# Optimization experiments

Measured on AMD Instinct MI355X. Metric: run time of the kernel, lower is better.

The kernel has to match this reference:

```python
import jax, jax.numpy as jnp
import numpy as np

EPS = 1e-12  # matches torch F.normalize default eps (clamp_min)
B, C, N = 32, 512, 4096
K_CLUSTERS, G_CLUSTERS = 64, 8
T_CLUSTERS = K_CLUSTERS + G_CLUSTERS  # 72
H_ATTN = T_CLUSTERS // 4  # 18


def _l2norm(v, axis):
    return v / jnp.maximum(jnp.linalg.norm(v, axis=axis, keepdims=True), EPS)


def setup_inputs() -> dict:
    key = jax.random.key(0)
    ks = jax.random.split(key, 6)
    x = jax.random.normal(ks[0], (B, C, N), dtype=jnp.float32)
    centroids = jax.random.normal(ks[1], (T_CLUSTERS, C), dtype=jnp.float32) * 0.01
    # 1x1 Conv2d(C -> T) == dense [T, C] weight + bias
    conv_w = jax.random.normal(ks[2], (T_CLUSTERS, C), dtype=jnp.float32) / np.sqrt(C).astype(np.float32)
    conv_b = jnp.zeros((T_CLUSTERS,), dtype=jnp.float32)
    ghost_weights = jnp.ones((G_CLUSTERS,), dtype=jnp.float32) * 0.1
    w1 = jax.random.normal(ks[3], (H_ATTN, T_CLUSTERS), dtype=jnp.float32) / np.sqrt(T_CLUSTERS).astype(np.float32)
    b1 = jnp.zeros((H_ATTN,), dtype=jnp.float32)
    w2 = jax.random.normal(ks[4], (T_CLUSTERS, H_ATTN), dtype=jnp.float32) / np.sqrt(H_ATTN).astype(np.float32)
    b2 = jnp.zeros((T_CLUSTERS,), dtype=jnp.float32)
    return {"x": x, "centroids": centroids, "conv_w": conv_w, "conv_b": conv_b,
            "ghost_weights": ghost_weights, "w1": w1, "b1": b1, "w2": w2, "b2": b2}


def reference(x, centroids, conv_w, conv_b, ghost_weights, w1, b1, w2, b2):
    # x: [B, C, N] -> L2 normalize over channel dim
    xn = _l2norm(x, axis=1)
    # 1x1 conv -> soft assignment logits [B, T, N], softmax over clusters
    logits = jnp.einsum('kc,bcn->bkn', conv_w, xn) + conv_b[None, :, None]
    assign = jax.nn.softmax(logits, axis=1)
    # residual aggregation, algebraically fused:
    # vlad[b,k,c] = sum_n a[b,k,n]*x[b,c,n] - centroid[k,c]*sum_n a[b,k,n]
    agg = jnp.einsum('bkn,bcn->bkc', assign, xn)
    mass = assign.sum(axis=-1)  # [B, T]
    vlad = agg - centroids[None, :, :] * mass[:, :, None]
    # ghost cluster down-weighting
    gw = jax.nn.softmax(ghost_weights)
    vlad = vlad.at[:, K_CLUSTERS:, :].multiply(gw[None, :, None])
    # attention over clusters: mean over C -> MLP -> softmax over clusters
    scores = vlad.mean(axis=-1)  # [B, T]
    h = jax.nn.relu(scores @ w1.T + b1)
    attn = jax.nn.softmax(h @ w2.T + b2, axis=1)
    vlad = vlad * attn[:, :, None]
    # intra-cluster L2 norm, drop ghosts, flatten, global L2 norm
    vlad = _l2norm(vlad, axis=2)
    vlad = vlad[:, :K_CLUSTERS, :].reshape(vlad.shape[0], -1)
    return _l2norm(vlad, axis=1)
```

## Files before the change

kernel.cpp:

```cpp
#include <hip/hip_runtime.h>
#include <hip/hip_bf16.h>

#define B_ 32
#define C_ 512
#define N_ 4096
#define T_ 72
#define K_ 64
#define KP 80
#define EPSF 1e-12f

typedef unsigned short u16;
typedef unsigned int u32;
typedef __attribute__((ext_vector_type(8))) short bf16x8;
typedef __attribute__((ext_vector_type(4))) float f32x4;

__device__ __forceinline__ u16 f2bf(float v) {
    __hip_bfloat16 h = __float2bfloat16(v);
    return *reinterpret_cast<u16*>(&h);
}

__global__ __launch_bounds__(256) void k_prep(
    const float* __restrict__ conv_w, const float* __restrict__ conv_b,
    u16* __restrict__ Wp, float* __restrict__ bp)
{
    const int idx = blockIdx.x * 256 + threadIdx.x;
    if (idx < KP * C_) {
        const int k = idx >> 9, c = idx & (C_ - 1);
        Wp[idx] = f2bf(k < T_ ? conv_w[k * C_ + c] : 0.f);
    } else if (idx < KP * C_ + KP) {
        const int j = idx - KP * C_;
        bp[j] = (j < T_) ? conv_b[j] : -1e30f;
    }
}

#define AN 64
#define ACH 256
__global__ __launch_bounds__(256) void k_assign(
    const float* __restrict__ x, const u16* __restrict__ Wp,
    const float* __restrict__ bp, u16* __restrict__ assignp,
    float* __restrict__ mass)
{
    __shared__ u16   xt[AN][264];
    __shared__ float red[AN][9];
    __shared__ float linv[AN];

    const int t  = threadIdx.x;
    const int b  = blockIdx.y;
    const int n0 = blockIdx.x * AN;

    const int np = t & 31;
    const int cg = t >> 5;
    const float* xb = x + (size_t)b * C_ * N_ + n0 + 2 * np;

    const int lane = t & 63, w = t >> 6;
    const int q = lane >> 4, nl = lane & 15;

    f32x4 acc[5];
    #pragma unroll
    for (int mt = 0; mt < 5; ++mt) acc[mt] = (f32x4)0.f;

    float ss0 = 0.f, ss1 = 0.f;

    #pragma unroll 1
    for (int half = 0; half < 2; ++half) {
        const int cbase = half * ACH;
        #pragma unroll 4
        for (int ci = 0; ci < 32; ++ci) {
            const int c = cg * 32 + ci;
            const float2 v = *(const float2*)(xb + (size_t)(cbase + c) * N_);
            ss0 = fmaf(v.x, v.x, ss0);
            ss1 = fmaf(v.y, v.y, ss1);
            xt[2 * np][c]     = f2bf(v.x);
            xt[2 * np + 1][c] = f2bf(v.y);
        }
        if (half == 1) {
            red[2 * np][cg]     = ss0;
            red[2 * np + 1][cg] = ss1;
        }
        __syncthreads();
        if (half == 1 && t < AN) {
            float s = 0.f;
            #pragma unroll
            for (int j = 0; j < 8; ++j) s += red[t][j];
            linv[t] = 1.0f / fmaxf(sqrtf(s), EPSF);
        }
        const u16* wrow = Wp + (size_t)nl * C_ + cbase + q * 8;
        #pragma unroll
        for (int ks = 0; ks < ACH / 32; ++ks) {
            const bf16x8 bf = *(const bf16x8*)(&xt[16 * w + nl][ks * 32 + q * 8]);
            #pragma unroll
            for (int mt = 0; mt < 5; ++mt) {
                const bf16x8 af = *(const bf16x8*)(wrow + (size_t)(mt * 16) * C_ + ks * 32);
                acc[mt] = __builtin_amdgcn_mfma_f32_16x16x32_bf16(af, bf, acc[mt], 0, 0, 0);
            }
        }
        __syncthreads();
    }

    const float invn  = linv[16 * w + nl];
    const int   nglob = n0 + 16 * w + nl;

    float lg[5][4];
    #pragma unroll
    for (int mt = 0; mt < 5; ++mt)
        #pragma unroll
        for (int r = 0; r < 4; ++r)
            lg[mt][r] = acc[mt][r] * invn + bp[mt * 16 + q * 4 + r];

    float mx = -1e30f;
    #pragma unroll
    for (int mt = 0; mt < 5; ++mt)
        #pragma unroll
        for (int r = 0; r < 4; ++r) mx = fmaxf(mx, lg[mt][r]);
    mx = fmaxf(mx, __shfl_xor(mx, 16, 64));
    mx = fmaxf(mx, __shfl_xor(mx, 32, 64));

    float s = 0.f;
    #pragma unroll
    for (int mt = 0; mt < 5; ++mt)
        #pragma unroll
        for (int r = 0; r < 4; ++r) {
            lg[mt][r] = __expf(lg[mt][r] - mx);
            s += lg[mt][r];
        }
    s += __shfl_xor(s, 16, 64);
    s += __shfl_xor(s, 32, 64);
    const float rs = 1.0f / s;

    #pragma unroll
    for (int mt = 0; mt < 4; ++mt)
        #pragma unroll
        for (int r = 0; r < 4; ++r) {
            const float a = lg[mt][r] * rs;
            float msum = a;
            msum += __shfl_xor(msum, 1, 64);
            msum += __shfl_xor(msum, 2, 64);
            msum += __shfl_xor(msum, 4, 64);
            msum += __shfl_xor(msum, 8, 64);
            const int k = mt * 16 + q * 4 + r;
            if (nl == 0) atomicAdd(&mass[b * K_ + k], msum);
            assignp[((size_t)b * K_ + k) * N_ + nglob] = f2bf(a * invn);
        }
}

#define GBK 64
#define NCH 4
__global__ __launch_bounds__(256) void k_agg(
    const float* __restrict__ x, const u16* __restrict__ assignp,
    float* __restrict__ out)
{
    __shared__ u16 At[K_][72];
    __shared__ u16 Bt[K_][72];

    const int t  = threadIdx.x;
    const int b  = blockIdx.z;
    const int nc0 = blockIdx.y * (N_ / NCH);
    const int c0  = blockIdx.x * 64;

    const int lane = t & 63, w = t >> 6;
    const int q = lane >> 4, nl = lane & 15;

    f32x4 acc[4];
    #pragma unroll
    for (int mt = 0; mt < 4; ++mt) acc[mt] = (f32x4)0.f;

    const u16*   ab = assignp + (size_t)b * K_ * N_;
    const float* xb = x + (size_t)b * C_ * N_;

    const int au = t & 7,  ar = t >> 3;
    const int bp2 = t & 31, bc = t >> 5;

    #pragma unroll 1
    for (int n0 = nc0; n0 < nc0 + N_ / NCH; n0 += GBK) {
        __syncthreads();
        #pragma unroll
        for (int p = 0; p < 2; ++p) {
            const int r = ar + 32 * p;
            *(uint4*)(&At[r][au * 8]) =
                *(const uint4*)(ab + (size_t)r * N_ + n0 + au * 8);
        }
        #pragma unroll
        for (int p = 0; p < 8; ++p) {
            const int c = bc + 8 * p;
            const float2 v = *(const float2*)(xb + (size_t)(c0 + c) * N_ + n0 + 2 * bp2);
            const u32 pk = (u32)f2bf(v.x) | ((u32)f2bf(v.y) << 16);
            *(u32*)(&Bt[c][2 * bp2]) = pk;
        }
        __syncthreads();
        #pragma unroll
        for (int kk = 0; kk < 2; ++kk) {
            const bf16x8 bf = *(const bf16x8*)(&Bt[16 * w + nl][kk * 32 + q * 8]);
            #pragma unroll
            for (int mt = 0; mt < 4; ++mt) {
                const bf16x8 af = *(const bf16x8*)(&At[mt * 16 + nl][kk * 32 + q * 8]);
                acc[mt] = __builtin_amdgcn_mfma_f32_16x16x32_bf16(af, bf, acc[mt], 0, 0, 0);
            }
        }
    }

    float* ob = out + (size_t)b * K_ * C_;
    const int c = c0 + 16 * w + nl;
    #pragma unroll
    for (int mt = 0; mt < 4; ++mt)
        #pragma unroll
        for (int r = 0; r < 4; ++r)
            atomicAdd(&ob[(size_t)(mt * 16 + q * 4 + r) * C_ + c], acc[mt][r]);
}

__device__ __forceinline__ float block_reduce_sum_256(float v) {
    #pragma unroll
    for (int o = 32; o > 0; o >>= 1) v += __shfl_down(v, o, 64);
    __shared__ float wsh[4];
    const int lane = threadIdx.x & 63, wid = threadIdx.x >> 6;
    if (lane == 0) wsh[wid] = v;
    __syncthreads();
    float r = 0.f;
    if (threadIdx.x == 0) r = wsh[0] + wsh[1] + wsh[2] + wsh[3];
    return r;
}

__global__ __launch_bounds__(256) void k_rnorm(
    const float* __restrict__ agg, const float* __restrict__ centroids,
    const float* __restrict__ mass, float* __restrict__ rnorm,
    float* __restrict__ gsum)
{
    const int k = blockIdx.x, b = blockIdx.y;
    const float mk = mass[b * K_ + k];
    const float* p  = agg + ((size_t)b * K_ + k) * C_;
    const float* cb = centroids + k * C_;
    float s = 0.f;
    #pragma unroll 2
    for (int i = threadIdx.x; i < C_; i += 256) {
        const float v = fmaf(-cb[i], mk, p[i]);
        s = fmaf(v, v, s);
    }
    const float ss = block_reduce_sum_256(s);
    if (threadIdx.x == 0) {
        const float rn = fmaxf(sqrtf(ss), EPSF);
        rnorm[b * K_ + k] = rn;
        atomicAdd(gsum + b, ss / (rn * rn));
    }
}

__global__ __launch_bounds__(256) void k_final(
    float* __restrict__ out, const float* __restrict__ centroids,
    const float* __restrict__ mass, const float* __restrict__ rnorm,
    const float* __restrict__ gsum)
{
    const size_t i4 = ((size_t)blockIdx.x * 256 + threadIdx.x) * 4;
    const int b = (int)(i4 >> 15);
    const int k = (int)((i4 >> 9) & 63);
    const int c = (int)(i4 & 511);
    const float gn = fmaxf(sqrtf(gsum[b]), EPSF);
    const float sc = 1.0f / (rnorm[b * K_ + k] * gn);
    const float mk = mass[b * K_ + k];
    float4 v  = *(const float4*)(out + i4);
    const float4 cv = *(const float4*)(centroids + k * C_ + c);
    v.x = fmaf(-cv.x, mk, v.x) * sc;
    v.y = fmaf(-cv.y, mk, v.y) * sc;
    v.z = fmaf(-cv.z, mk, v.z) * sc;
    v.w = fmaf(-cv.w, mk, v.w) * sc;
    *(float4*)(out + i4) = v;
}

extern "C" void kernel_launch(void* const* d_in, const int* in_sizes, int n_in,
                              void* d_out, int out_size, void* d_ws, size_t ws_size,
                              hipStream_t stream) {
    const float* x         = (const float*)d_in[0];
    const float* centroids = (const float*)d_in[1];
    const float* conv_w    = (const float*)d_in[2];
    const float* conv_b    = (const float*)d_in[3];

    float* out = (float*)d_out;
    char*  ws  = (char*)d_ws;

    u16*   assignp = (u16*)ws;
    u16*   Wp      = (u16*)(ws + 16777216);
    float* bpad    = (float*)(ws + 16777216 + 81920);
    float* mass    = (float*)(ws + 16777216 + 81920 + 320);
    float* rnorm   = mass + B_ * K_;
    float* gsum    = rnorm + B_ * K_;

    hipMemsetAsync(mass, 0, B_ * K_ * sizeof(float), stream);
    hipMemsetAsync(gsum, 0, B_ * sizeof(float), stream);
    hipMemsetAsync(out, 0, (size_t)out_size * sizeof(float), stream);

    k_prep<<<dim3((KP * C_ + KP + 255) / 256), 256, 0, stream>>>(conv_w, conv_b, Wp, bpad);
    k_assign<<<dim3(N_ / AN, B_), 256, 0, stream>>>(x, Wp, bpad, assignp, mass);
    k_agg<<<dim3(C_ / 64, NCH, B_), 256, 0, stream>>>(x, assignp, out);
    k_rnorm<<<dim3(K_, B_), 256, 0, stream>>>(out, centroids, mass, rnorm, gsum);
    k_final<<<(out_size / 4 + 255) / 256, 256, 0, stream>>>(out, centroids, mass, rnorm, gsum);
}
```

Baseline: 544.8 us.

## Make assign and aggregation kernels wave-private with register prefetch and no block barriers

k_assign now has each wave load its own 16-column slice of x with float4 loads into a per-wave LDS tile. It reduces squared norms with wave shuffles instead of a block-shared reduction, and prefetches the next channel quarter into registers while the MFMAs run. k_agg drops the shared assignment tile, reads assignment fragments straight from global memory, keeps x per wave in LDS with register double-buffering, and doubles the N split to 8 chunks for more blocks. Together these aim to remove __syncthreads stalls and overlap global loads with compute. The cost is more redundant global reads of assignments across waves and more atomics on the output.

Measured after the change: 571.6 us. 1.05x slower.

```diff
diff --git a/kernel.cpp b/kernel.cpp
--- a/kernel.cpp
+++ b/kernel.cpp
@@ -34,71 +34,89 @@
 }
 
 #define AN 64
-#define ACH 256
 __global__ __launch_bounds__(256) void k_assign(
     const float* __restrict__ x, const u16* __restrict__ Wp,
     const float* __restrict__ bp, u16* __restrict__ assignp,
     float* __restrict__ mass)
 {
-    __shared__ u16   xt[AN][264];
-    __shared__ float red[AN][9];
-    __shared__ float linv[AN];
+    __shared__ u16 xw[4][16][136];
 
     const int t  = threadIdx.x;
     const int b  = blockIdx.y;
     const int n0 = blockIdx.x * AN;
 
-    const int np = t & 31;
-    const int cg = t >> 5;
-    const float* xb = x + (size_t)b * C_ * N_ + n0 + 2 * np;
-
     const int lane = t & 63, w = t >> 6;
-    const int q = lane >> 4, nl = lane & 15;
+    const int q  = lane >> 4, nl = lane & 15;
+    const int nq = lane & 3,  cg = lane >> 2;
+
+    const float* xb = x + (size_t)b * C_ * N_ + n0 + 16 * w + 4 * nq;
 
     f32x4 acc[5];
     #pragma unroll
     for (int mt = 0; mt < 5; ++mt) acc[mt] = (f32x4)0.f;
-
-    float ss0 = 0.f, ss1 = 0.f;
-
-    #pragma unroll 1
-    for (int half = 0; half < 2; ++half) {
-        const int cbase = half * ACH;
-        #pragma unroll 4
-        for (int ci = 0; ci < 32; ++ci) {
-            const int c = cg * 32 + ci;
-            const float2 v = *(const float2*)(xb + (size_t)(cbase + c) * N_);
-            ss0 = fmaf(v.x, v.x, ss0);
-            ss1 = fmaf(v.y, v.y, ss1);
-            xt[2 * np][c]     = f2bf(v.x);
-            xt[2 * np + 1][c] = f2bf(v.y);
-        }
-        if (half == 1) {
-            red[2 * np][cg]     = ss0;
-            red[2 * np + 1][cg] = ss1;
-        }
-        __syncthreads();
-        if (half == 1 && t < AN) {
-            float s = 0.f;
+    float ss[4] = {0.f, 0.f, 0.f, 0.f};
+
+    float4 va[4], vc[4];
+    #pragma unroll
+    for (int ci = 0; ci < 4; ++ci) {
+        const size_t coff = (size_t)(32 * ci + 2 * cg) * N_;
+        va[ci] = *(const float4*)(xb + coff);
+        vc[ci] = *(const float4*)(xb + coff + N_);
+    }
+
+    #pragma unroll
+    for (int qtr = 0; qtr < 4; ++qtr) {
+        #pragma unroll
+        for (int ci = 0; ci < 4; ++ci) {
+            const int cl = 32 * ci + 2 * cg;
+            const float4 v0 = va[ci], v1 = vc[ci];
+            ss[0] = fmaf(v0.x, v0.x, ss[0]); ss[0] = fmaf(v1.x, v1.x, ss[0]);
+            ss[1] = fmaf(v0.y, v0.y, ss[1]); ss[1] = fmaf(v1.y, v1.y, ss[1]);
+            ss[2] = fmaf(v0.z, v0.z, ss[2]); ss[2] = fmaf(v1.z, v1.z, ss[2]);
+            ss[3] = fmaf(v0.w, v0.w, ss[3]); ss[3] = fmaf(v1.w, v1.w, ss[3]);
+            *(u32*)&xw[w][4 * nq + 0][cl] = (u32)f2bf(v0.x) | ((u32)f2bf(v1.x) << 16);
+            *(u32*)&xw[w][4 * nq + 1][cl] = (u32)f2bf(v0.y) | ((u32)f2bf(v1.y) << 16);
+            *(u32*)&xw[w][4 * nq + 2][cl] = (u32)f2bf(v0.z) | ((u32)f2bf(v1.z) << 16);
+            *(u32*)&xw[w][4 * nq + 3][cl] = (u32)f2bf(v0.w) | ((u32)f2bf(v1.w) << 16);
+        }
+        if (qtr < 3) {
             #pragma unroll
-            for (int j = 0; j < 8; ++j) s += red[t][j];
-            linv[t] = 1.0f / fmaxf(sqrtf(s), EPSF);
-        }
-        const u16* wrow = Wp + (size_t)nl * C_ + cbase + q * 8;
-        #pragma unroll
-        for (int ks = 0; ks < ACH / 32; ++ks) {
-            const bf16x8 bf = *(const bf16x8*)(&xt[16 * w + nl][ks * 32 + q * 8]);
+            for (int ci = 0; ci < 4; ++ci) {
+                const size_t coff = (size_t)((qtr + 1) * 128 + 32 * ci + 2 * cg) * N_;
+                va[ci] = *(const float4*)(xb + coff);
+                vc[ci] = *(const float4*)(xb + coff + N_);
+            }
+        }
+        const u16* wq = Wp + (size_t)nl * C_ + qtr * 128 + q * 8;
+        #pragma unroll
+        for (int ks = 0; ks < 4; ++ks) {
+            const bf16x8 bfr = *(const bf16x8*)&xw[w][nl][ks * 32 + q * 8];
             #pragma unroll
             for (int mt = 0; mt < 5; ++mt) {
-                const bf16x8 af = *(const bf16x8*)(wrow + (size_t)(mt * 16) * C_ + ks * 32);
-                acc[mt] = __builtin_amdgcn_mfma_f32_16x16x32_bf16(af, bf, acc[mt], 0, 0, 0);
+                const bf16x8 af = *(const bf16x8*)(wq + (size_t)(mt * 16) * C_ + ks * 32);
+                acc[mt] = __builtin_amdgcn_mfma_f32_16x16x32_bf16(af, bfr, acc[mt], 0, 0, 0);
             }
         }
-        __syncthreads();
-    }
-
-    const float invn  = linv[16 * w + nl];
-    const int   nglob = n0 + 16 * w + nl;
+    }
+
+    #pragma unroll
+    for (int j = 0; j < 4; ++j) {
+        ss[j] += __shfl_xor(ss[j], 4, 64);
+        ss[j] += __shfl_xor(ss[j], 8, 64);
+        ss[j] += __shfl_xor(ss[j], 16, 64);
+        ss[j] += __shfl_xor(ss[j], 32, 64);
+    }
+    float inv[4];
+    #pragma unroll
+    for (int j = 0; j < 4; ++j) inv[j] = 1.0f / fmaxf(sqrtf(ss[j]), EPSF);
+
+    const int src = nl >> 2;
+    const float i0 = __shfl(inv[0], src, 64);
+    const float i1 = __shfl(inv[1], src, 64);
+    const float i2 = __shfl(inv[2], src, 64);
+    const float i3 = __shfl(inv[3], src, 64);
+    const float invn = (nl & 2) ? ((nl & 1) ? i3 : i2) : ((nl & 1) ? i1 : i0);
+    const int nglob = n0 + 16 * w + nl;
 
     float lg[5][4];
     #pragma unroll
@@ -144,13 +162,12 @@
 }
 
 #define GBK 64
-#define NCH 4
+#define NCH 8
 __global__ __launch_bounds__(256) void k_agg(
     const float* __restrict__ x, const u16* __restrict__ assignp,
     float* __restrict__ out)
 {
-    __shared__ u16 At[K_][72];
-    __shared__ u16 Bt[K_][72];
+    __shared__ u16 Bt[4][16][72];
 
     const int t  = threadIdx.x;
     const int b  = blockIdx.z;
@@ -159,41 +176,42 @@
 
     const int lane = t & 63, w = t >> 6;
     const int q = lane >> 4, nl = lane & 15;
+    const int nq16 = lane & 15, cj = lane >> 4;
 
     f32x4 acc[4];
     #pragma unroll
     for (int mt = 0; mt < 4; ++mt) acc[mt] = (f32x4)0.f;
 
-    const u16*   ab = assignp + (size_t)b * K_ * N_;
-    const float* xb = x + (size_t)b * C_ * N_;
-
-    const int au = t & 7,  ar = t >> 3;
-    const int bp2 = t & 31, bc = t >> 5;
+    const u16*   ab = assignp + (size_t)b * K_ * N_ + (size_t)nl * N_ + q * 8;
+    const float* xb = x + ((size_t)b * C_ + c0 + 16 * w) * N_ + 4 * nq16;
+
+    float4 vb[4];
+    #pragma unroll
+    for (int p = 0; p < 4; ++p)
+        vb[p] = *(const float4*)(xb + (size_t)(4 * p + cj) * N_ + nc0);
 
     #pragma unroll 1
     for (int n0 = nc0; n0 < nc0 + N_ / NCH; n0 += GBK) {
-        __syncthreads();
-        #pragma unroll
-        for (int p = 0; p < 2; ++p) {
-            const int r = ar + 32 * p;
-            *(uint4*)(&At[r][au * 8]) =
-                *(const uint4*)(ab + (size_t)r * N_ + n0 + au * 8);
-        }
-        #pragma unroll
-        for (int p = 0; p < 8; ++p) {
-            const int c = bc + 8 * p;
-            const float2 v = *(const float2*)(xb + (size_t)(c0 + c) * N_ + n0 + 2 * bp2);
-            const u32 pk = (u32)f2bf(v.x) | ((u32)f2bf(v.y) << 16);
-            *(u32*)(&Bt[c][2 * bp2]) = pk;
-        }
-        __syncthreads();
+        #pragma unroll
+        for (int p = 0; p < 4; ++p) {
+            const float4 v = vb[p];
+            uint2 pk;
+            pk.x = (u32)f2bf(v.x) | ((u32)f2bf(v.y) << 16);
+            pk.y = (u32)f2bf(v.z) | ((u32)f2bf(v.w) << 16);
+            *(uint2*)&Bt[w][4 * p + cj][4 * nq16] = pk;
+        }
+        if (n0 + GBK < nc0 + N_ / NCH) {
+            #pragma unroll
+            for (int p = 0; p < 4; ++p)
+                vb[p] = *(const float4*)(xb + (size_t)(4 * p + cj) * N_ + n0 + GBK);
+        }
         #pragma unroll
         for (int kk = 0; kk < 2; ++kk) {
-            const bf16x8 bf = *(const bf16x8*)(&Bt[16 * w + nl][kk * 32 + q * 8]);
+            const bf16x8 bfr = *(const bf16x8*)&Bt[w][nl][kk * 32 + q * 8];
             #pragma unroll
             for (int mt = 0; mt < 4; ++mt) {
-                const bf16x8 af = *(const bf16x8*)(&At[mt * 16 + nl][kk * 32 + q * 8]);
-                acc[mt] = __builtin_amdgcn_mfma_f32_16x16x32_bf16(af, bf, acc[mt], 0, 0, 0);
+                const bf16x8 af = *(const bf16x8*)(ab + (size_t)(mt * 16) * N_ + n0 + kk * 32);
+                acc[mt] = __builtin_amdgcn_mfma_f32_16x16x32_bf16(af, bfr, acc[mt], 0, 0, 0);
             }
         }
     }
```
